# Kernel optimization log

Measured on AMD Instinct MI355X. Metric: run time of the kernel, lower is better.

The kernel has to match this reference:

```python
import jax, jax.numpy as jnp
import numpy as np

N_SRC, N_DST, E, D = 100000, 100000, 1250000, 64


def setup_inputs() -> dict:
    key = jax.random.key(0)
    k1, k2, k3, k4 = jax.random.split(key, 4)
    h_src = jax.random.normal(k1, (N_SRC, D), dtype=jnp.float32)
    mask = jax.random.uniform(k2, (E,), dtype=jnp.float32)
    src_idx = jax.random.randint(k3, (E,), 0, N_SRC, dtype=jnp.int32)
    dst_idx = jax.random.randint(k4, (E,), 0, N_DST, dtype=jnp.int32)
    return {"h_src": h_src, "mask": mask, "src_idx": src_idx,
            "dst_idx": dst_idx, "n_dst": N_DST}


def reference(h_src, mask, src_idx, dst_idx, n_dst):
    # h_src: [N_src, D]; mask: [E]; src_idx/dst_idx: [E]
    n_src = h_src.shape[0]
    ones = jnp.ones(src_idx.shape[0], dtype=h_src.dtype)
    # out-degree normalization of source features (deg^-0.5, clamped at 1)
    out_deg = jnp.clip(jax.ops.segment_sum(ones, src_idx, num_segments=n_src), 1.0, None)
    feat_src = h_src * (out_deg ** -0.5)[:, None]
    # message = src feature * edge mask; reduce = segment-sum at destination
    msgs = feat_src[src_idx] * mask[:, None]            # [E, D]
    rst = jax.ops.segment_sum(msgs, dst_idx, num_segments=n_dst)  # [N_dst, D]
    # in-degree normalization of result
    in_deg = jnp.clip(jax.ops.segment_sum(ones, dst_idx, num_segments=n_dst), 1.0, None)
    return rst * (in_deg ** -0.5)[:, None]
```

## Files before the change

### kernel.cpp

```cpp
#include <hip/hip_runtime.h>
#include <hip/hip_fp16.h>

#define D 64
#define TILE_W 64
#define LOG_TW 6
#define MAXT 1600
#define NB 256
#define CAPE 1024
#define BIG 1024
#define MQ 511.0f
#define CMAX 4928
#define NCH 4

__device__ inline void block_exscan_1024(const int* __restrict__ hist,
                                         int* __restrict__ loc,
                                         int n, int* __restrict__ wsum) {
    int tid = threadIdx.x;
    int lane = tid & 63, w = tid >> 6;
    int i0 = 2 * tid, i1 = i0 + 1;
    int v0 = (i0 < n) ? hist[i0] : 0;
    int v1 = (i1 < n) ? hist[i1] : 0;
    int v = v0 + v1;
    int incl = v;
    for (int off = 1; off < 64; off <<= 1) {
        int u = __shfl_up(incl, off, 64);
        if (lane >= off) incl += u;
    }
    if (lane == 63) wsum[w] = incl;
    __syncthreads();
    if (w == 0 && lane < 16) {
        int x = wsum[lane];
        int inc2 = x;
        for (int off = 1; off < 16; off <<= 1) {
            int u = __shfl_up(inc2, off, 64);
            if (lane >= off) inc2 += u;
        }
        wsum[lane] = inc2 - x;
    }
    __syncthreads();
    int excl = wsum[w] + incl - v;
    if (i0 < n) loc[i0] = excl;
    if (i1 < n) loc[i1] = excl + v0;
    if (tid == 1023) loc[n] = excl + v;
    __syncthreads();
}

__global__ __launch_bounds__(1024) void p3_sortplace(
        const float* __restrict__ mask,
        const int* __restrict__ src_idx,
        const int* __restrict__ dst_idx,
        int E, int Td, int Ts, int C,
        unsigned int* __restrict__ csrD,
        unsigned char* __restrict__ srcb,
        int* __restrict__ locD,
        int* __restrict__ locS) {
    __shared__ int histD[MAXT];
    __shared__ int histS[MAXT];
    __shared__ int curD[MAXT + 1];
    __shared__ int curS[MAXT + 1];
    __shared__ int wsum[16];
    __shared__ unsigned int  ebuf[CMAX];
    __shared__ unsigned short dbuf[CMAX];
    int b = blockIdx.x;
    int lo = b * C, hi = min(E, lo + C);
    int cnt = hi - lo;
    for (int t = threadIdx.x; t < Td; t += 1024) histD[t] = 0;
    for (int t = threadIdx.x; t < Ts; t += 1024) histS[t] = 0;
    __syncthreads();
    for (int i = threadIdx.x; i < cnt; i += 1024) {
        int e = lo + i;
        int s = src_idx[e], d = dst_idx[e];
        unsigned int q = min((unsigned int)(mask[e] * MQ + 0.5f), 511u);
        ebuf[i] = ((unsigned int)s << 15) |
                  ((unsigned int)(d & (TILE_W - 1)) << 9) | q;
        dbuf[i] = (unsigned short)(d >> LOG_TW);
        atomicAdd(&histD[d >> LOG_TW], 1);
        atomicAdd(&histS[s >> LOG_TW], 1);
    }
    __syncthreads();
    block_exscan_1024(histD, curD, Td, wsum);
    block_exscan_1024(histS, curS, Ts, wsum);
    for (int t = threadIdx.x; t <= Td; t += 1024) locD[(size_t)b * (Td + 1) + t] = curD[t];
    for (int t = threadIdx.x; t <= Ts; t += 1024) locS[(size_t)b * (Ts + 1) + t] = curS[t];
    __syncthreads();
    for (int i = threadIdx.x; i < cnt; i += 1024) {
        unsigned int w = ebuf[i];
        int pd = atomicAdd(&curD[dbuf[i]], 1);
        csrD[lo + pd] = w;
        unsigned int s = w >> 15;
        int ps = atomicAdd(&curS[s >> LOG_TW], 1);
        srcb[lo + ps] = (unsigned char)(s & (TILE_W - 1));
    }
}

__global__ void p3bc_feat(const unsigned char* __restrict__ srcb,
                          const int* __restrict__ locS,
                          const float* __restrict__ h_src,
                          int Ts, int C, int n_src,
                          uint2* __restrict__ feat) {
    __shared__ int hist[TILE_W];
    __shared__ float rs[TILE_W];
    int t = blockIdx.x;
    int tid = threadIdx.x;
    if (tid < TILE_W) hist[tid] = 0;
    __syncthreads();
    for (int b = tid; b < NB; b += blockDim.x) {
        int base = b * C;
        int s0 = locS[(size_t)b * (Ts + 1) + t];
        int s1 = locS[(size_t)b * (Ts + 1) + t + 1];
        for (int i = base + s0; i < base + s1; ++i)
            atomicAdd(&hist[srcb[i]], 1);
    }
    __syncthreads();
    if (tid < TILE_W) rs[tid] = rsqrtf((float)max(hist[tid], 1));
    __syncthreads();
    int base_row = t * TILE_W;
    int nrows = min(TILE_W, n_src - base_row);
    int total = nrows * 16;
    for (int i = tid; i < total; i += blockDim.x) {
        int r = i >> 4, sub = i & 15;
        float4 v = ((const float4*)h_src)[(size_t)(base_row + r) * 16 + sub];
        float sc2 = rs[r];
        __half2 lo2 = __halves2half2(__float2half(v.x * sc2), __float2half(v.y * sc2));
        __half2 hi2 = __halves2half2(__float2half(v.z * sc2), __float2half(v.w * sc2));
        union { __half2 h2[2]; uint2 u; } pk;
        pk.h2[0] = lo2; pk.h2[1] = hi2;
        feat[(size_t)(base_row + r) * 16 + sub] = pk.u;
    }
}

__global__ __launch_bounds__(256) void p4_gather(
        const uint2* __restrict__ feat,
        const unsigned int* __restrict__ csrD,
        const int* __restrict__ locD,
        int Td, int C, int n_dst,
        float* __restrict__ out) {
    __shared__ unsigned int ebuf2[CAPE];
    __shared__ int2 segs[NB];
    __shared__ int hist2[TILE_W * NCH];
    __shared__ int dstart2[TILE_W * NCH];
    __shared__ int cur2[TILE_W * NCH];
    __shared__ int wsum[4];
    __shared__ int totsh;
    int t = blockIdx.x;
    int tid = threadIdx.x;
    hist2[tid] = 0;
    {
        int s0 = locD[(size_t)tid * (Td + 1) + t];
        int s1 = locD[(size_t)tid * (Td + 1) + t + 1];
        segs[tid] = make_int2(tid * C + s0, tid * C + s1);
    }
    __syncthreads();

    {
        int2 sg = segs[tid];
        for (int i = sg.x; i < sg.y; ++i) {
            unsigned int p = csrD[i];
            int key = (int)(((p >> 9) & (TILE_W - 1)) << 2) | (int)(p >> 30);
            atomicAdd(&hist2[key], 1);
        }
    }
    __syncthreads();

    {
        int lane = tid & 63, w = tid >> 6;
        int v = hist2[tid];
        int incl = v;
        for (int off = 1; off < 64; off <<= 1) {
            int u = __shfl_up(incl, off, 64);
            if (lane >= off) incl += u;
        }
        if (lane == 63) wsum[w] = incl;
        __syncthreads();
        if (tid == 0) {
            int run = 0;
            for (int i = 0; i < 4; ++i) { int x = wsum[i]; wsum[i] = run; run += x; }
            totsh = run;
        }
        __syncthreads();
        int excl = wsum[w] + incl - v;
        dstart2[tid] = excl;
        cur2[tid]    = excl;
    }
    __syncthreads();
    int n_e = min(totsh, CAPE);

    {
        int2 sg = segs[tid];
        for (int i = sg.x; i < sg.y; ++i) {
            unsigned int p = csrD[i];
            int key = (int)(((p >> 9) & (TILE_W - 1)) << 2) | (int)(p >> 30);
            int pos = atomicAdd(&cur2[key], 1);
            ebuf2[min(pos, CAPE - 1)] = p;
        }
    }
    __syncthreads();

    int wid = tid >> 6, lane = tid & 63;
    int q = lane >> 4, sub = lane & 15;
    for (int k = 0; k < 16; ++k) {
        int d = wid * 16 + k;
        int dg = t * TILE_W + d;
        if (dg >= n_dst) continue;
        int st  = dstart2[d << 2];
        int end = (d < TILE_W - 1) ? dstart2[(d + 1) << 2] : totsh;
        int n = end - st;
        float4 a0 = make_float4(0.f, 0.f, 0.f, 0.f);
        float4 a1 = make_float4(0.f, 0.f, 0.f, 0.f);
        for (int j = 0; j < n; j += 8) {
            {
                bool val = (j + q) < n;
                unsigned int p = ebuf2[val ? min(st + j + q, CAPE - 1) : 0];
                float c = val ? (float)(p & 511u) * (1.0f / MQ) : 0.f;
                unsigned int row = p >> 15;
                uint2 f = feat[(size_t)row * 16 + sub];
                union { uint2 u; __half2 h2[2]; } pk; pk.u = f;
                float2 f0 = __half22float2(pk.h2[0]);
                float2 f1 = __half22float2(pk.h2[1]);
                a0.x += c * f0.x; a0.y += c * f0.y;
                a0.z += c * f1.x; a0.w += c * f1.y;
            }
            {
                bool val = (j + 4 + q) < n;
                unsigned int p = ebuf2[val ? min(st + j + 4 + q, CAPE - 1) : 0];
                float c = val ? (float)(p & 511u) * (1.0f / MQ) : 0.f;
                unsigned int row = p >> 15;
                uint2 f = feat[(size_t)row * 16 + sub];
                union { uint2 u; __half2 h2[2]; } pk; pk.u = f;
                float2 f0 = __half22float2(pk.h2[0]);
                float2 f1 = __half22float2(pk.h2[1]);
                a1.x += c * f0.x; a1.y += c * f0.y;
                a1.z += c * f1.x; a1.w += c * f1.y;
            }
        }
        float4 acc = make_float4(a0.x + a1.x, a0.y + a1.y, a0.z + a1.z, a0.w + a1.w);
        acc.x += __shfl_xor(acc.x, 16, 64); acc.x += __shfl_xor(acc.x, 32, 64);
        acc.y += __shfl_xor(acc.y, 16, 64); acc.y += __shfl_xor(acc.y, 32, 64);
        acc.z += __shfl_xor(acc.z, 16, 64); acc.z += __shfl_xor(acc.z, 32, 64);
        acc.w += __shfl_xor(acc.w, 16, 64); acc.w += __shfl_xor(acc.w, 32, 64);
        if (q == 0) {
            float rn = rsqrtf((float)max(n, 1));
            ((float4*)out)[(size_t)dg * 16 + sub] =
                make_float4(acc.x * rn, acc.y * rn, acc.z * rn, acc.w * rn);
        }
    }
}

__global__ void fill_kernel(const float* __restrict__ mask,
                            const int* __restrict__ src_idx,
                            const int* __restrict__ dst_idx,
                            int E,
                            int* __restrict__ out_deg,
                            int* __restrict__ cursor,
                            int2* __restrict__ sorted) {
    int i = blockIdx.x * blockDim.x + threadIdx.x;
    int stride = gridDim.x * blockDim.x;
    for (int e = i; e < E; e += stride) {
        int s = src_idx[e];
        int t = dst_idx[e];
        atomicAdd(&out_deg[s], 1);
        int pos = atomicAdd(&cursor[t], 1);
        if (pos < 64) {
            int2 m; m.x = s; m.y = __float_as_int(mask[e]);
            sorted[(size_t)t * 64 + pos] = m;
        }
    }
}

__global__ void gatherF_kernel(const float* __restrict__ h_src,
                               const int* __restrict__ out_deg,
                               const int* __restrict__ cursor,
                               const int2* __restrict__ sorted,
                               int n_dst,
                               float* __restrict__ out) {
    int wid  = threadIdx.x >> 6;
    int lane = threadIdx.x & 63;
    int t = blockIdx.x * (blockDim.x >> 6) + wid;
    if (t >= n_dst) return;
    int n = min(cursor[t], 64);
    int   s_mine = 0;
    float c_mine = 0.f;
    if (lane < n) {
        int2 m = sorted[(size_t)t * 64 + lane];
        s_mine = m.x;
        c_mine = __int_as_float(m.y) * rsqrtf((float)max(out_deg[m.x], 1));
    }
    float acc = 0.f;
    for (int j = 0; j < n; ++j) {
        int   s = __shfl(s_mine, j, 64);
        float c = __shfl(c_mine, j, 64);
        acc += c * h_src[(size_t)s * D + lane];
    }
    out[(size_t)t * D + lane] = acc * rsqrtf((float)max(n, 1));
}

extern "C" void kernel_launch(void* const* d_in, const int* in_sizes, int n_in,
                              void* d_out, int out_size, void* d_ws, size_t ws_size,
                              hipStream_t stream) {
    const float* h_src   = (const float*)d_in[0];
    const float* mask    = (const float*)d_in[1];
    const int*   src_idx = (const int*)d_in[2];
    const int*   dst_idx = (const int*)d_in[3];
    int n_src = in_sizes[0] / D;
    int E     = in_sizes[1];
    int n_dst = out_size / D;
    float* out = (float*)d_out;

    int Td = (n_dst + TILE_W - 1) / TILE_W;
    int Ts = (n_src + TILE_W - 1) / TILE_W;
    int C  = (E + NB - 1) / NB;

    auto al = [](size_t x) { return (x + 255) & ~(size_t)255; };
    size_t off_csr  = 0;
    size_t off_srcb = al(off_csr + (size_t)E * sizeof(unsigned int));
    size_t off_locD = al(off_srcb + (size_t)E);
    size_t off_locS = al(off_locD + (size_t)NB * (Td + 1) * sizeof(int));
    size_t off_feat = al(off_locS + (size_t)NB * (Ts + 1) * sizeof(int));
    size_t need     = off_feat + (size_t)n_src * D * sizeof(__half);

    if (ws_size >= need && Td <= MAXT && Ts <= MAXT && C <= CMAX &&
        n_src <= (1 << 17) && (D % 4) == 0) {
        unsigned int*  csrD = (unsigned int*)((char*)d_ws + off_csr);
        unsigned char* srcb = (unsigned char*)((char*)d_ws + off_srcb);
        int*           locD = (int*)((char*)d_ws + off_locD);
        int*           locS = (int*)((char*)d_ws + off_locS);
        uint2*         feat = (uint2*)((char*)d_ws + off_feat);

        p3_sortplace<<<NB, BIG, 0, stream>>>(mask, src_idx, dst_idx,
                                             E, Td, Ts, C, csrD, srcb, locD, locS);
        p3bc_feat<<<Ts, 256, 0, stream>>>(srcb, locS, h_src, Ts, C, n_src, feat);
        p4_gather<<<Td, 256, 0, stream>>>(feat, csrD, locD, Td, C, n_dst, out);
    } else {
        int*  out_deg = (int*)d_ws;
        int*  cursor  = out_deg + n_src;
        int2* sorted  = (int2*)(cursor + n_dst);
        hipMemsetAsync(d_ws, 0, (size_t)(n_src + n_dst) * sizeof(int), stream);
        fill_kernel<<<2048, 256, 0, stream>>>(mask, src_idx, dst_idx, E,
                                              out_deg, cursor, sorted);
        int blocks = (n_dst + 3) / 4;
        gatherF_kernel<<<blocks, 256, 0, stream>>>(h_src, out_deg, cursor, sorted,
                                                   n_dst, out);
    }
}
```

Baseline: 85.81 us.

## Double gather block to 512 threads and iterate edges by source chunk

Launches the destination gather kernel with 512 threads per block instead of 256. Two threads now share each segment during the histogram and placement passes, and the scan is restricted to the first 256 threads. Each wave now owns 8 destinations and holds their accumulators in registers while it walks the four source-chunk sub-ranges in order, so feature reads are grouped by source chunk for better locality. The cost is more registers per thread (eight float4 accumulators), a shorter 4-edge inner step with less memory-level parallelism per wave, and extra barriers in the idle threads.

```diff
diff --git a/kernel.cpp b/kernel.cpp
--- a/kernel.cpp
+++ b/kernel.cpp
@@ -129,7 +129,7 @@
     }
 }
 
-__global__ __launch_bounds__(256) void p4_gather(
+__global__ __launch_bounds__(512) void p4_gather(
         const uint2* __restrict__ feat,
         const unsigned int* __restrict__ csrD,
         const int* __restrict__ locD,
@@ -138,14 +138,13 @@
     __shared__ unsigned int ebuf2[CAPE];
     __shared__ int2 segs[NB];
     __shared__ int hist2[TILE_W * NCH];
-    __shared__ int dstart2[TILE_W * NCH];
+    __shared__ int dstart2[TILE_W * NCH + 1];
     __shared__ int cur2[TILE_W * NCH];
     __shared__ int wsum[4];
-    __shared__ int totsh;
     int t = blockIdx.x;
     int tid = threadIdx.x;
-    hist2[tid] = 0;
-    {
+    if (tid < TILE_W * NCH) hist2[tid] = 0;
+    if (tid < NB) {
         int s0 = locD[(size_t)tid * (Td + 1) + t];
         int s1 = locD[(size_t)tid * (Td + 1) + t + 1];
         segs[tid] = make_int2(tid * C + s0, tid * C + s1);
@@ -153,8 +152,9 @@
     __syncthreads();
 
     {
-        int2 sg = segs[tid];
-        for (int i = sg.x; i < sg.y; ++i) {
+        int b = tid >> 1;
+        int2 sg = segs[b];
+        for (int i = sg.x + (tid & 1); i < sg.y; i += 2) {
             unsigned int p = csrD[i];
             int key = (int)(((p >> 9) & (TILE_W - 1)) << 2) | (int)(p >> 30);
             atomicAdd(&hist2[key], 1);
@@ -162,7 +162,7 @@
     }
     __syncthreads();
 
-    {
+    if (tid < TILE_W * NCH) {
         int lane = tid & 63, w = tid >> 6;
         int v = hist2[tid];
         int incl = v;
@@ -175,19 +175,22 @@
         if (tid == 0) {
             int run = 0;
             for (int i = 0; i < 4; ++i) { int x = wsum[i]; wsum[i] = run; run += x; }
-            totsh = run;
+            dstart2[TILE_W * NCH] = run;
         }
         __syncthreads();
         int excl = wsum[w] + incl - v;
         dstart2[tid] = excl;
         cur2[tid]    = excl;
-    }
-    __syncthreads();
-    int n_e = min(totsh, CAPE);
+    } else {
+        __syncthreads();
+        __syncthreads();
+    }
+    __syncthreads();
 
     {
-        int2 sg = segs[tid];
-        for (int i = sg.x; i < sg.y; ++i) {
+        int b = tid >> 1;
+        int2 sg = segs[b];
+        for (int i = sg.x + (tid & 1); i < sg.y; i += 2) {
             unsigned int p = csrD[i];
             int key = (int)(((p >> 9) & (TILE_W - 1)) << 2) | (int)(p >> 30);
             int pos = atomicAdd(&cur2[key], 1);
@@ -198,50 +201,45 @@
 
     int wid = tid >> 6, lane = tid & 63;
     int q = lane >> 4, sub = lane & 15;
-    for (int k = 0; k < 16; ++k) {
-        int d = wid * 16 + k;
-        int dg = t * TILE_W + d;
-        if (dg >= n_dst) continue;
-        int st  = dstart2[d << 2];
-        int end = (d < TILE_W - 1) ? dstart2[(d + 1) << 2] : totsh;
-        int n = end - st;
-        float4 a0 = make_float4(0.f, 0.f, 0.f, 0.f);
-        float4 a1 = make_float4(0.f, 0.f, 0.f, 0.f);
-        for (int j = 0; j < n; j += 8) {
-            {
-                bool val = (j + q) < n;
-                unsigned int p = ebuf2[val ? min(st + j + q, CAPE - 1) : 0];
+    float4 acc[8];
+    #pragma unroll
+    for (int k = 0; k < 8; ++k) acc[k] = make_float4(0.f, 0.f, 0.f, 0.f);
+
+    for (int ch = 0; ch < NCH; ++ch) {
+        #pragma unroll
+        for (int k = 0; k < 8; ++k) {
+            int d = wid * 8 + k;
+            int st = dstart2[(d << 2) + ch];
+            int en = dstart2[(d << 2) + ch + 1];
+            for (int j = st; j < en; j += 4) {
+                bool val = (j + q) < en;
+                unsigned int p = ebuf2[val ? min(j + q, CAPE - 1) : 0];
                 float c = val ? (float)(p & 511u) * (1.0f / MQ) : 0.f;
                 unsigned int row = p >> 15;
                 uint2 f = feat[(size_t)row * 16 + sub];
                 union { uint2 u; __half2 h2[2]; } pk; pk.u = f;
                 float2 f0 = __half22float2(pk.h2[0]);
                 float2 f1 = __half22float2(pk.h2[1]);
-                a0.x += c * f0.x; a0.y += c * f0.y;
-                a0.z += c * f1.x; a0.w += c * f1.y;
+                acc[k].x += c * f0.x; acc[k].y += c * f0.y;
+                acc[k].z += c * f1.x; acc[k].w += c * f1.y;
             }
-            {
-                bool val = (j + 4 + q) < n;
-                unsigned int p = ebuf2[val ? min(st + j + 4 + q, CAPE - 1) : 0];
-                float c = val ? (float)(p & 511u) * (1.0f / MQ) : 0.f;
-                unsigned int row = p >> 15;
-                uint2 f = feat[(size_t)row * 16 + sub];
-                union { uint2 u; __half2 h2[2]; } pk; pk.u = f;
-                float2 f0 = __half22float2(pk.h2[0]);
-                float2 f1 = __half22float2(pk.h2[1]);
-                a1.x += c * f0.x; a1.y += c * f0.y;
-                a1.z += c * f1.x; a1.w += c * f1.y;
-            }
-        }
-        float4 acc = make_float4(a0.x + a1.x, a0.y + a1.y, a0.z + a1.z, a0.w + a1.w);
-        acc.x += __shfl_xor(acc.x, 16, 64); acc.x += __shfl_xor(acc.x, 32, 64);
-        acc.y += __shfl_xor(acc.y, 16, 64); acc.y += __shfl_xor(acc.y, 32, 64);
-        acc.z += __shfl_xor(acc.z, 16, 64); acc.z += __shfl_xor(acc.z, 32, 64);
-        acc.w += __shfl_xor(acc.w, 16, 64); acc.w += __shfl_xor(acc.w, 32, 64);
-        if (q == 0) {
+        }
+    }
+
+    #pragma unroll
+    for (int k = 0; k < 8; ++k) {
+        int d = wid * 8 + k;
+        int dg = t * TILE_W + d;
+        float4 a = acc[k];
+        a.x += __shfl_xor(a.x, 16, 64); a.x += __shfl_xor(a.x, 32, 64);
+        a.y += __shfl_xor(a.y, 16, 64); a.y += __shfl_xor(a.y, 32, 64);
+        a.z += __shfl_xor(a.z, 16, 64); a.z += __shfl_xor(a.z, 32, 64);
+        a.w += __shfl_xor(a.w, 16, 64); a.w += __shfl_xor(a.w, 32, 64);
+        if (q == 0 && dg < n_dst) {
+            int n = dstart2[(d + 1) << 2] - dstart2[d << 2];
             float rn = rsqrtf((float)max(n, 1));
             ((float4*)out)[(size_t)dg * 16 + sub] =
-                make_float4(acc.x * rn, acc.y * rn, acc.z * rn, acc.w * rn);
+                make_float4(a.x * rn, a.y * rn, a.z * rn, a.w * rn);
         }
     }
 }
@@ -329,7 +327,7 @@
         p3_sortplace<<<NB, BIG, 0, stream>>>(mask, src_idx, dst_idx,
                                              E, Td, Ts, C, csrD, srcb, locD, locS);
         p3bc_feat<<<Ts, 256, 0, stream>>>(srcb, locS, h_src, Ts, C, n_src, feat);
-        p4_gather<<<Td, 256, 0, stream>>>(feat, csrD, locD, Td, C, n_dst, out);
+        p4_gather<<<Td, 512, 0, stream>>>(feat, csrD, locD, Td, C, n_dst, out);
     } else {
         int*  out_deg = (int*)d_ws;
         int*  cursor  = out_deg + n_src;
```

Measured after the change: 89.73 us. 1.05x slower.
